# Performance work log

Measured on AMD Instinct MI355X. Metric: run time of the kernel, lower is better.

Reference implementation:

```python
import jax, jax.numpy as jnp
import numpy as np

N_NODES = 50000
N_EDGES_UND = 400000
N_GRAPHS = 128
LATENT = 64
OUT_DIM = 64
NODE_F = 64
EDGE_F = 32
MAX_LV = 3


def setup_inputs() -> dict:
    key = jax.random.key(0)
    ks = jax.random.split(key, 12)
    rng = np.random.default_rng(0)
    # Build consistent directed edge list: each undirected pair (u,v) yields
    # directed edges e (u->v) and e+E_und (v->u); rev maps each to its twin.
    u = rng.integers(0, N_NODES, size=N_EDGES_UND)
    v = rng.integers(0, N_NODES, size=N_EDGES_UND)
    src = jnp.asarray(np.concatenate([u, v]), dtype=jnp.int32)
    dst = jnp.asarray(np.concatenate([v, u]), dtype=jnp.int32)
    e = np.arange(N_EDGES_UND)
    rev = jnp.asarray(np.concatenate([e + N_EDGES_UND, e]), dtype=jnp.int32)
    graph_ids = jnp.sort(jax.random.randint(ks[0], (N_NODES,), 0, N_GRAPHS)).astype(jnp.int32)
    s = 0.05
    return {
        'node_feat': jax.random.normal(ks[1], (N_NODES, NODE_F), jnp.float32),
        'edge_feat': jax.random.normal(ks[2], (2 * N_EDGES_UND, EDGE_F), jnp.float32),
        'src': src, 'dst': dst, 'rev': rev,
        'graph_ids': graph_ids, 'n_graphs': N_GRAPHS,
        'Wn': jax.random.normal(ks[3], (NODE_F, LATENT), jnp.float32) * s,
        'bn': jnp.zeros((LATENT,), jnp.float32),
        'We': jax.random.normal(ks[4], (EDGE_F, LATENT), jnp.float32) * s,
        'be': jnp.zeros((LATENT,), jnp.float32),
        'Wc': jax.random.normal(ks[5], (LATENT, LATENT), jnp.float32) * s,
        'bc': jnp.zeros((LATENT,), jnp.float32),
        'Wo': jax.random.normal(ks[6], (LATENT, OUT_DIM), jnp.float32) * s,
        'bo': jnp.zeros((OUT_DIM,), jnp.float32),
    }


def reference(node_feat, edge_feat, src, dst, rev, graph_ids, n_graphs,
              Wn, bn, We, be, Wc, bc, Wo, bo):
    n_nodes = node_feat.shape[0]
    # w_n2l / w_e2l
    input_node_linear = node_feat @ Wn + bn                  # [N, D]
    input_edge_linear = edge_feat @ We + be                  # [E, D]
    # n2e spmm: each directed edge gathers its source node's row
    input_message = input_edge_linear + input_node_linear[src]  # [E, D]
    cur = jax.nn.relu(input_message)
    # loopy BP: e2e spmm = (sum of messages into src node) - reverse-edge message
    for _ in range(MAX_LV):
        node_agg = jax.ops.segment_sum(cur, dst, num_segments=n_nodes)  # [N, D]
        e2epool = node_agg[src] - cur[rev]                              # [E, D]
        cur = jax.nn.relu(e2epool @ Wc + bc + input_message)
    # e2n spmm: sum incoming edge messages per node
    e2npool = jax.ops.segment_sum(cur, dst, num_segments=n_nodes)       # [N, D]
    hidden_msg = jax.nn.relu(e2npool)
    reluact = jax.nn.relu(hidden_msg @ Wo + bo)                         # [N, out]
    # subg spmm: sum node outputs per graph
    y = jax.ops.segment_sum(reluact, graph_ids, num_segments=n_graphs)  # [G, out]
    return jax.nn.relu(y)
```

## Files before the change

kernel.cpp:

```cpp
#include <hip/hip_runtime.h>


#define NN 50000
#define NE 800000
#define NG 128
#define D 64
#define LDE 36
#define LDW 66
#define LDO 72

typedef unsigned short u16;
typedef unsigned int u32;
typedef __bf16 bf16x8 __attribute__((ext_vector_type(8)));
typedef float f32x4 __attribute__((ext_vector_type(4)));

__device__ __forceinline__ float b2f(u16 u){ u32 x=((u32)u)<<16; float f; __builtin_memcpy(&f,&x,4); return f; }
__device__ __forceinline__ u16 f2b(float f){ u32 x; __builtin_memcpy(&x,&f,4); x += 0x7fffu + ((x>>16)&1u); return (u16)(x>>16); }
__device__ __forceinline__ u32 pack2(float a, float b){ return (u32)f2b(a) | ((u32)f2b(b)<<16); }
__device__ __forceinline__ void unpack8(uint4 v, float* o){
  o[0]=b2f((u16)(v.x&0xffffu)); o[1]=b2f((u16)(v.x>>16));
  o[2]=b2f((u16)(v.y&0xffffu)); o[3]=b2f((u16)(v.y>>16));
  o[4]=b2f((u16)(v.z&0xffffu)); o[5]=b2f((u16)(v.z>>16));
  o[6]=b2f((u16)(v.w&0xffffu)); o[7]=b2f((u16)(v.w>>16));
}

__global__ __launch_bounds__(256) void k_inl(const float* __restrict__ nf, const float* __restrict__ Wn,
                                             const float* __restrict__ bn, u16* __restrict__ inlb){
  __shared__ float w[D*D];
  for (int i=threadIdx.x;i<D*D;i+=256) w[i]=Wn[i];
  __syncthreads();
  const int d = threadIdx.x&63;
  const int n = blockIdx.x*4 + (threadIdx.x>>6);
  if (n>=NN) return;
  float v = bn[d];
  const float* row = nf + (size_t)n*D;
  #pragma unroll 8
  for (int k=0;k<D;k++) v += row[k]*w[k*D+d];
  inlb[(size_t)n*D+d] = f2b(v);
}

__global__ __launch_bounds__(256) void k_im(const float* __restrict__ ef, const float* __restrict__ We,
                                            const float* __restrict__ be, const u16* __restrict__ inlb,
                                            const int* __restrict__ src, const int* __restrict__ perm,
                                            u16* __restrict__ imP){
  __shared__ __align__(16) u16 efs[64*LDE];
  __shared__ __align__(16) u16 wts[64*LDE];
  __shared__ float os[64*68];
  const int t = threadIdx.x;
  const int ebase = blockIdx.x*64;
  {
    int n=t&63, k0=(t>>6)*8;
    #pragma unroll
    for (int j=0;j<8;j++) wts[n*LDE + k0 + j] = f2b(We[(k0+j)*D + n]);
  }
  {
    int e=t>>2, k0=(t&3)*8;
    const float* p = ef + (size_t)(ebase+e)*32 + k0;
    float4 v0=*(const float4*)p, v1=*(const float4*)(p+4);
    uint4 pk = make_uint4(pack2(v0.x,v0.y),pack2(v0.z,v0.w),pack2(v1.x,v1.y),pack2(v1.z,v1.w));
    *(uint4*)&efs[e*LDE + k0] = pk;
  }
  __syncthreads();
  {
    int w=t>>6, lane=t&63, q=lane>>4, mr=lane&15;
    int rowb=w*16;
    bf16x8 A = *(const bf16x8*)&efs[(rowb+mr)*LDE + q*8];
    #pragma unroll
    for (int nt=0;nt<4;nt++){
      bf16x8 B = *(const bf16x8*)&wts[(nt*16+mr)*LDE + q*8];
      f32x4 acc = {0.f,0.f,0.f,0.f};
      acc = __builtin_amdgcn_mfma_f32_16x16x32_bf16(A,B,acc,0,0,0);
      #pragma unroll
      for (int r=0;r<4;r++) os[(rowb+q*4+r)*68 + nt*16+mr] = acc[r];
    }
  }
  __syncthreads();
  {
    int e=t>>2, d0=(t&3)*16;
    const size_t eg = (size_t)(ebase+e);
    const int s = src[eg], ps = perm[eg];
    const u16* ip = inlb + (size_t)s*D + d0;
    uint4 iv0 = *(const uint4*)ip, iv1 = *(const uint4*)(ip+8);
    float il[16]; unpack8(iv0,il); unpack8(iv1,il+8);
    float x[16];
    #pragma unroll
    for (int j=0;j<16;j++) x[j] = os[e*68 + d0 + j] + be[d0+j] + il[j];
    uint4 p0 = make_uint4(pack2(x[0],x[1]),pack2(x[2],x[3]),pack2(x[4],x[5]),pack2(x[6],x[7]));
    uint4 p1 = make_uint4(pack2(x[8],x[9]),pack2(x[10],x[11]),pack2(x[12],x[13]),pack2(x[14],x[15]));
    u16* op = imP + (size_t)ps*D + d0;
    *(uint4*)op = p0; *(uint4*)(op+8) = p1;
  }
}

template<int MODE>
__global__ __launch_bounds__(256) void k_iter(const u16* __restrict__ imP, const u16* __restrict__ revIn,
      const float* __restrict__ naW_in, const float* __restrict__ Wc, const float* __restrict__ bc,
      const int* __restrict__ srcP, const int* __restrict__ prevP, const int* __restrict__ nodeP,
      u16* __restrict__ revOut, float* __restrict__ naW_out){
  __shared__ __align__(16) u16 xs[64*LDW];
  __shared__ __align__(16) u16 wts[64*LDW];
  __shared__ __align__(16) u16 os[64*LDO];
  __shared__ int nid[64];
  const int t = threadIdx.x;
  const size_t sbase = (size_t)blockIdx.x*64;
  {
    int n=t&63, k0=(t>>6)*16;
    #pragma unroll
    for (int j=0;j<16;j++) wts[n*LDW + k0 + j] = f2b(Wc[(k0+j)*D + n]);
  }
  if (t < 64) nid[t] = nodeP[sbase + t];
  {
    const int e = t>>2, d0 = (t&3)*16;
    const size_t slot = sbase + e;
    const u16* ip = imP + slot*D + d0;
    uint4 r0 = *(const uint4*)ip;
    uint4 r1 = *(const uint4*)(ip+8);
    float x[16];
    unpack8(r0, x); unpack8(r1, x+8);
    if (MODE == 1){
      const int sp = srcP[slot];
      const u16* cp = revIn + slot*D + d0;
      uint4 c0 = *(const uint4*)cp, c1 = *(const uint4*)(cp+8);
      const float* np_ = naW_in + (size_t)sp*D + d0;
      float4 a0=*(const float4*)np_,     a1=*(const float4*)(np_+4);
      float4 a2=*(const float4*)(np_+8), a3=*(const float4*)(np_+12);
      float nv[16] = {a0.x,a0.y,a0.z,a0.w, a1.x,a1.y,a1.z,a1.w,
                      a2.x,a2.y,a2.z,a2.w, a3.x,a3.y,a3.z,a3.w};
      float cv[16];
      unpack8(c0,cv); unpack8(c1,cv+8);
      #pragma unroll
      for (int j=0;j<16;j++) x[j] += nv[j] - cv[j] + bc[d0+j];
    }
    #pragma unroll
    for (int j=0;j<16;j++) x[j] = x[j]>0.f ? x[j] : 0.f;
    uint4 p0 = make_uint4(pack2(x[0],x[1]),pack2(x[2],x[3]),pack2(x[4],x[5]),pack2(x[6],x[7]));
    uint4 p1 = make_uint4(pack2(x[8],x[9]),pack2(x[10],x[11]),pack2(x[12],x[13]),pack2(x[14],x[15]));
    u16* q = &xs[e*LDW + d0];
    *(uint4*)q = p0; *(uint4*)(q+8) = p1;
  }
  __syncthreads();
  {
    const int w=t>>6, lane=t&63, q=lane>>4, mr=lane&15;
    const int rowb = w*16;
    bf16x8 A0 = *(const bf16x8*)&xs[(rowb+mr)*LDW + q*8];
    bf16x8 A1 = *(const bf16x8*)&xs[(rowb+mr)*LDW + 32 + q*8];
    #pragma unroll
    for (int nt=0;nt<4;nt++){
      bf16x8 B0 = *(const bf16x8*)&wts[(nt*16+mr)*LDW + q*8];
      bf16x8 B1 = *(const bf16x8*)&wts[(nt*16+mr)*LDW + 32 + q*8];
      f32x4 acc = {0.f,0.f,0.f,0.f};
      acc = __builtin_amdgcn_mfma_f32_16x16x32_bf16(A0,B0,acc,0,0,0);
      acc = __builtin_amdgcn_mfma_f32_16x16x32_bf16(A1,B1,acc,0,0,0);
      #pragma unroll
      for (int r=0;r<4;r++) os[(rowb+q*4+r)*LDO + nt*16 + mr] = f2b(acc[r]);
    }
    const int lr = lane>>2, cc = lane&3;
    const int tgt = prevP[sbase + rowb + lr];
    u16* gp = revOut + (size_t)tgt*D + cc*16;
    *(uint4*)gp     = *(const uint4*)&os[(rowb+lr)*LDO + cc*16];
    *(uint4*)(gp+8) = *(const uint4*)&os[(rowb+lr)*LDO + cc*16 + 8];
    const int d = lane;
    float acc = 0.f;
    int curn = nid[rowb];
    #pragma unroll 4
    for (int r = rowb; r < rowb+16; ++r){
      int n = nid[r];
      if (n != curn){
        atomicAdd(&naW_out[(size_t)curn*D + d], acc);
        curn = n; acc = 0.f;
      }
      acc += b2f(os[r*LDO + d]);
    }
    atomicAdd(&naW_out[(size_t)curn*D + d], acc);
  }
}

__global__ __launch_bounds__(256) void k_last(const u16* __restrict__ imP, const u16* __restrict__ revIn,
      const float* __restrict__ naW_in, const float* __restrict__ bc,
      const int* __restrict__ srcP, const int* __restrict__ nodeP,
      float* __restrict__ e2n){
  __shared__ __align__(16) u16 xs[64*LDW];
  __shared__ int nid[64];
  const int t = threadIdx.x;
  const size_t sbase = (size_t)blockIdx.x*64;
  if (t < 64) nid[t] = nodeP[sbase + t];
  {
    const int e = t>>2, d0 = (t&3)*16;
    const size_t slot = sbase + e;
    const u16* ip = imP + slot*D + d0;
    uint4 r0 = *(const uint4*)ip, r1 = *(const uint4*)(ip+8);
    float x[16];
    unpack8(r0, x); unpack8(r1, x+8);
    const int sp = srcP[slot];
    const u16* cp = revIn + slot*D + d0;
    uint4 c0 = *(const uint4*)cp, c1 = *(const uint4*)(cp+8);
    const float* np_ = naW_in + (size_t)sp*D + d0;
    float4 a0=*(const float4*)np_,     a1=*(const float4*)(np_+4);
    float4 a2=*(const float4*)(np_+8), a3=*(const float4*)(np_+12);
    float nv[16] = {a0.x,a0.y,a0.z,a0.w, a1.x,a1.y,a1.z,a1.w,
                    a2.x,a2.y,a2.z,a2.w, a3.x,a3.y,a3.z,a3.w};
    float cv[16];
    unpack8(c0,cv); unpack8(c1,cv+8);
    #pragma unroll
    for (int j=0;j<16;j++){ x[j] += nv[j] - cv[j] + bc[d0+j]; x[j] = x[j]>0.f ? x[j] : 0.f; }
    uint4 p0 = make_uint4(pack2(x[0],x[1]),pack2(x[2],x[3]),pack2(x[4],x[5]),pack2(x[6],x[7]));
    uint4 p1 = make_uint4(pack2(x[8],x[9]),pack2(x[10],x[11]),pack2(x[12],x[13]),pack2(x[14],x[15]));
    u16* q = &xs[e*LDW + d0];
    *(uint4*)q = p0; *(uint4*)(q+8) = p1;
  }
  __syncthreads();
  {
    const int d = t&63, g = t>>6;
    float acc = 0.f;
    int curn = nid[g*16];
    #pragma unroll 4
    for (int r = g*16; r < g*16+16; ++r){
      int n = nid[r];
      if (n != curn){
        atomicAdd(&e2n[(size_t)curn*D + d], acc);
        curn = n; acc = 0.f;
      }
      acc += b2f(xs[r*LDW + d]);
    }
    atomicAdd(&e2n[(size_t)curn*D + d], acc);
  }
}

__global__ void k_hist(const int* __restrict__ dst, int* __restrict__ cnt){
  int e = blockIdx.x*256 + threadIdx.x;
  atomicAdd(&cnt[dst[e]], 1);
}
__global__ __launch_bounds__(1024) void k_scan1(const int* __restrict__ cnt, int* __restrict__ outv,
                                                int* __restrict__ bsums, int n){
  __shared__ int sh[1024];
  int i = blockIdx.x*1024 + threadIdx.x;
  int v = (i<n)? cnt[i] : 0;
  sh[threadIdx.x]=v;
  __syncthreads();
  for (int off=1; off<1024; off<<=1){
    int tv = (threadIdx.x>=(unsigned)off)? sh[threadIdx.x-off] : 0;
    __syncthreads();
    sh[threadIdx.x] += tv;
    __syncthreads();
  }
  if (i<n) outv[i] = sh[threadIdx.x] - v;
  if (threadIdx.x==1023) bsums[blockIdx.x] = sh[1023];
}
__global__ void k_scan2(int* bsums, int nb, int* tot){
  if (threadIdx.x==0 && blockIdx.x==0){
    int run=0;
    for (int b=0;b<nb;b++){ int v=bsums[b]; bsums[b]=run; run+=v; }
    *tot = run;
  }
}
__global__ __launch_bounds__(1024) void k_scan3(int* __restrict__ off, int* __restrict__ cur,
                                                const int* __restrict__ bsums, int n){
  int i = blockIdx.x*1024 + threadIdx.x;
  if (i<n){ int v = off[i] + bsums[blockIdx.x]; off[i]=v; cur[i]=v; }
}
__global__ void k_fill(const int* __restrict__ dst, const int* __restrict__ src,
                       int* __restrict__ cur, int* __restrict__ perm,
                       int* __restrict__ srcP, int* __restrict__ nodeP){
  int e = blockIdx.x*256 + threadIdx.x;
  int d = dst[e];
  int pos = atomicAdd(&cur[d], 1);
  perm[e] = pos;
  srcP[pos] = src[e];
  nodeP[pos] = d;
}
__global__ void k_prev(const int* __restrict__ rev, const int* __restrict__ perm, int* __restrict__ prevP){
  int e = blockIdx.x*256 + threadIdx.x;
  prevP[perm[e]] = perm[rev[e]];
}

__global__ __launch_bounds__(256) void k_final(const float* __restrict__ e2n, const float* __restrict__ Wo,
                                               const float* __restrict__ bo, const int* __restrict__ gid,
                                               float* __restrict__ yacc){
  __shared__ float w[D*D];
  for (int i=threadIdx.x;i<D*D;i+=256) w[i]=Wo[i];
  __syncthreads();
  const int d = threadIdx.x&63, sub = threadIdx.x>>6;
  const int n0 = blockIdx.x*32 + sub*8;
  const float bod = bo[d];
  float acc=0.f; int curg=-1;
  for (int i=0;i<8;i++){
    int n=n0+i;
    if (n>=NN) break;
    int g = gid[n];
    if (g!=curg){ if (curg>=0) atomicAdd(&yacc[curg*D+d], acc); curg=g; acc=0.f; }
    float v=bod;
    const float* er = e2n + (size_t)n*D;
    #pragma unroll 8
    for (int k=0;k<D;k++){ float h=er[k]; h = h>0.f?h:0.f; v += h*w[k*D+d]; }
    acc += (v>0.f ? v : 0.f);
  }
  if (curg>=0) atomicAdd(&yacc[curg*D+d], acc);
}
__global__ void k_out(const float* __restrict__ yacc, float* __restrict__ outp){
  int i = blockIdx.x*256 + threadIdx.x;
  if (i<NG*D){ float v=yacc[i]; outp[i]= v>0.f?v:0.f; }
}

static constexpr size_t SZ_E   = (size_t)NE*D*2;
static constexpr size_t SZ_NF4 = (size_t)NN*D*4;
static constexpr size_t SZ_NB  = (size_t)NN*D*2;
static constexpr size_t OFF_IMP  = 0;
static constexpr size_t OFF_RVA  = SZ_E;
static constexpr size_t OFF_RVB  = 2*SZ_E;
static constexpr size_t OFF_NA0  = 3*SZ_E;
static constexpr size_t OFF_NA1  = OFF_NA0 + SZ_NF4;
static constexpr size_t OFF_E2N  = OFF_NA1 + SZ_NF4;
static constexpr size_t OFF_INL  = OFF_E2N + SZ_NF4;
static constexpr size_t OFF_COFF = OFF_INL + SZ_NB;
static constexpr size_t OFF_CCUR = OFF_COFF + 200064;
static constexpr size_t OFF_PERM = OFF_CCUR + 200064;
static constexpr size_t OFF_SRCP = OFF_PERM + (size_t)NE*4;
static constexpr size_t OFF_PRVP = OFF_SRCP + (size_t)NE*4;
static constexpr size_t OFF_NODP = OFF_PRVP + (size_t)NE*4;
static constexpr size_t OFF_BS   = OFF_NODP + (size_t)NE*4;
static constexpr size_t OFF_YACC = OFF_BS + 256;

extern "C" void kernel_launch(void* const* d_in, const int* in_sizes, int n_in,
                              void* d_out, int out_size, void* d_ws, size_t ws_size,
                              hipStream_t stream) {
  const float* node_feat = (const float*)d_in[0];
  const float* edge_feat = (const float*)d_in[1];
  const int*   src       = (const int*)d_in[2];
  const int*   dst       = (const int*)d_in[3];
  const int*   rev       = (const int*)d_in[4];
  const int*   gid       = (const int*)d_in[5];
  const float* Wn = (const float*)d_in[7];
  const float* bn = (const float*)d_in[8];
  const float* We = (const float*)d_in[9];
  const float* be = (const float*)d_in[10];
  const float* Wc = (const float*)d_in[11];
  const float* bc = (const float*)d_in[12];
  const float* Wo = (const float*)d_in[13];
  const float* bo = (const float*)d_in[14];

  char* ws = (char*)d_ws;
  u16*   imP     = (u16*)(ws + OFF_IMP);
  u16*   revA    = (u16*)(ws + OFF_RVA);
  u16*   revB    = (u16*)(ws + OFF_RVB);
  float* naW0    = (float*)(ws + OFF_NA0);
  float* naW1    = (float*)(ws + OFF_NA1);
  float* e2n     = (float*)(ws + OFF_E2N);
  u16*   inlb    = (u16*)(ws + OFF_INL);
  int*   csr_off = (int*)(ws + OFF_COFF);
  int*   csr_cur = (int*)(ws + OFF_CCUR);
  int*   perm    = (int*)(ws + OFF_PERM);
  int*   srcP    = (int*)(ws + OFF_SRCP);
  int*   prevP   = (int*)(ws + OFF_PRVP);
  int*   nodeP   = (int*)(ws + OFF_NODP);
  int*   bsums   = (int*)(ws + OFF_BS);
  float* yacc    = (float*)(ws + OFF_YACC);

  hipMemsetAsync(csr_cur, 0, NN*sizeof(int), stream);
  hipMemsetAsync(yacc, 0, NG*D*sizeof(float), stream);

  k_hist <<<NE/256, 256, 0, stream>>>(dst, csr_cur);
  k_scan1<<<49, 1024, 0, stream>>>(csr_cur, csr_off, bsums, NN);
  k_scan2<<<1, 64, 0, stream>>>(bsums, 49, csr_off + NN);
  k_scan3<<<49, 1024, 0, stream>>>(csr_off, csr_cur, bsums, NN);
  k_fill <<<NE/256, 256, 0, stream>>>(dst, src, csr_cur, perm, srcP, nodeP);
  k_prev <<<NE/256, 256, 0, stream>>>(rev, perm, prevP);

  k_inl<<<NN/4, 256, 0, stream>>>(node_feat, Wn, bn, inlb);
  k_im <<<NE/64, 256, 0, stream>>>(edge_feat, We, be, inlb, src, perm, imP);

  hipMemsetAsync(naW0, 0, SZ_NF4, stream);
  k_iter<0><<<NE/64, 256, 0, stream>>>(imP, revA, naW0, Wc, bc, srcP, prevP, nodeP, revA, naW0);
  hipMemsetAsync(naW1, 0, SZ_NF4, stream);
  k_iter<1><<<NE/64, 256, 0, stream>>>(imP, revA, naW0, Wc, bc, srcP, prevP, nodeP, revB, naW1);
  hipMemsetAsync(naW0, 0, SZ_NF4, stream);
  k_iter<1><<<NE/64, 256, 0, stream>>>(imP, revB, naW1, Wc, bc, srcP, prevP, nodeP, revA, naW0);
  hipMemsetAsync(e2n, 0, SZ_NF4, stream);
  k_last<<<NE/64, 256, 0, stream>>>(imP, revA, naW0, bc, srcP, nodeP, e2n);

  k_final<<<(NN+31)/32, 256, 0, stream>>>(e2n, Wo, bo, gid, yacc);
  k_out<<<(NG*D)/256, 256, 0, stream>>>(yacc, (float*)d_out);
}
```

Before: 710.3 us.

## Pretranspose weights, bf16 node aggregates, multi-tile iter blocks, merge memsets and scans

Weights Wc and We are transposed and converted to bf16 once in a prep kernel instead of in every block. Each k_iter block now processes four 64-edge tiles, amortising the weight staging. The fp32 node aggregates are converted to a bf16 copy before each gather, halving the bytes of the random reads. Several memsets are merged into one by reordering the workspace, k_scan2 is folded into k_scan3 with a wave reduction, and some barriers are removed because each wave now uses only its own rows. This adds extra conversion kernels, lowers the precision of the aggregates, and the removed barrier in k_im is questionable: each thread reads os rows written by other waves' MFMA results.

```diff
diff --git a/kernel.cpp b/kernel.cpp
--- a/kernel.cpp
+++ b/kernel.cpp
@@ -24,6 +24,23 @@
   o[6]=b2f((u16)(v.w&0xffffu)); o[7]=b2f((u16)(v.w>>16));
 }
 
+__global__ __launch_bounds__(256) void k_prep(const float* __restrict__ Wc, const float* __restrict__ We,
+                                              u16* __restrict__ wcT, u16* __restrict__ weT){
+  int i = blockIdx.x*256 + threadIdx.x;
+  if (i < 4096){ int n=i>>6, k=i&63; wcT[i] = f2b(Wc[k*D+n]); }
+  int j = i - 4096;
+  if (j >= 0 && j < 2048){ int n=j>>5, k=j&31; weT[j] = f2b(We[k*D+n]); }
+}
+
+template<int ZERO>
+__global__ __launch_bounds__(256) void k_cvt(const float* __restrict__ srcv, u16* __restrict__ dstb,
+                                             float* __restrict__ zbuf){
+  size_t i = (size_t)(blockIdx.x*256 + threadIdx.x)*4;
+  float4 v = *(const float4*)(srcv + i);
+  *(uint2*)(dstb + i) = make_uint2(pack2(v.x,v.y), pack2(v.z,v.w));
+  if (ZERO) *(float4*)(zbuf + i) = make_float4(0.f,0.f,0.f,0.f);
+}
+
 __global__ __launch_bounds__(256) void k_inl(const float* __restrict__ nf, const float* __restrict__ Wn,
                                              const float* __restrict__ bn, u16* __restrict__ inlb){
   __shared__ float w[D*D];
@@ -39,7 +56,7 @@
   inlb[(size_t)n*D+d] = f2b(v);
 }
 
-__global__ __launch_bounds__(256) void k_im(const float* __restrict__ ef, const float* __restrict__ We,
+__global__ __launch_bounds__(256) void k_im(const float* __restrict__ ef, const u16* __restrict__ weT,
                                             const float* __restrict__ be, const u16* __restrict__ inlb,
                                             const int* __restrict__ src, const int* __restrict__ perm,
                                             u16* __restrict__ imP){
@@ -50,8 +67,7 @@
   const int ebase = blockIdx.x*64;
   {
     int n=t&63, k0=(t>>6)*8;
-    #pragma unroll
-    for (int j=0;j<8;j++) wts[n*LDE + k0 + j] = f2b(We[(k0+j)*D + n]);
+    *(uint4*)&wts[n*LDE + k0] = *(const uint4*)(weT + n*32 + k0);
   }
   {
     int e=t>>2, k0=(t&3)*8;
@@ -74,7 +90,6 @@
       for (int r=0;r<4;r++) os[(rowb+q*4+r)*68 + nt*16+mr] = acc[r];
     }
   }
-  __syncthreads();
   {
     int e=t>>2, d0=(t&3)*16;
     const size_t eg = (size_t)(ebase+e);
@@ -94,7 +109,7 @@
 
 template<int MODE>
 __global__ __launch_bounds__(256) void k_iter(const u16* __restrict__ imP, const u16* __restrict__ revIn,
-      const float* __restrict__ naW_in, const float* __restrict__ Wc, const float* __restrict__ bc,
+      const u16* __restrict__ naWb, const u16* __restrict__ wcT, const float* __restrict__ bc,
       const int* __restrict__ srcP, const int* __restrict__ prevP, const int* __restrict__ nodeP,
       u16* __restrict__ revOut, float* __restrict__ naW_out){
   __shared__ __align__(16) u16 xs[64*LDW];
@@ -102,127 +117,129 @@
   __shared__ __align__(16) u16 os[64*LDO];
   __shared__ int nid[64];
   const int t = threadIdx.x;
-  const size_t sbase = (size_t)blockIdx.x*64;
-  {
-    int n=t&63, k0=(t>>6)*16;
-    #pragma unroll
-    for (int j=0;j<16;j++) wts[n*LDW + k0 + j] = f2b(Wc[(k0+j)*D + n]);
-  }
-  if (t < 64) nid[t] = nodeP[sbase + t];
-  {
-    const int e = t>>2, d0 = (t&3)*16;
-    const size_t slot = sbase + e;
-    const u16* ip = imP + slot*D + d0;
-    uint4 r0 = *(const uint4*)ip;
-    uint4 r1 = *(const uint4*)(ip+8);
-    float x[16];
-    unpack8(r0, x); unpack8(r1, x+8);
-    if (MODE == 1){
-      const int sp = srcP[slot];
-      const u16* cp = revIn + slot*D + d0;
-      uint4 c0 = *(const uint4*)cp, c1 = *(const uint4*)(cp+8);
-      const float* np_ = naW_in + (size_t)sp*D + d0;
-      float4 a0=*(const float4*)np_,     a1=*(const float4*)(np_+4);
-      float4 a2=*(const float4*)(np_+8), a3=*(const float4*)(np_+12);
-      float nv[16] = {a0.x,a0.y,a0.z,a0.w, a1.x,a1.y,a1.z,a1.w,
-                      a2.x,a2.y,a2.z,a2.w, a3.x,a3.y,a3.z,a3.w};
-      float cv[16];
-      unpack8(c0,cv); unpack8(c1,cv+8);
+  const int lane = t&63, w = t>>6;
+  {
+    const int k0 = w*16;
+    *(uint4*)&wts[lane*LDW + k0]     = *(const uint4*)(wcT + lane*64 + k0);
+    *(uint4*)&wts[lane*LDW + k0 + 8] = *(const uint4*)(wcT + lane*64 + k0 + 8);
+  }
+  const int e = t>>2, d0 = (t&3)*16;
+  float bcr[16];
+  if (MODE == 1){
+    float4 b0=*(const float4*)(bc+d0),   b1=*(const float4*)(bc+d0+4);
+    float4 b2=*(const float4*)(bc+d0+8), b3=*(const float4*)(bc+d0+12);
+    bcr[0]=b0.x;bcr[1]=b0.y;bcr[2]=b0.z;bcr[3]=b0.w; bcr[4]=b1.x;bcr[5]=b1.y;bcr[6]=b1.z;bcr[7]=b1.w;
+    bcr[8]=b2.x;bcr[9]=b2.y;bcr[10]=b2.z;bcr[11]=b2.w; bcr[12]=b3.x;bcr[13]=b3.y;bcr[14]=b3.z;bcr[15]=b3.w;
+  }
+  __syncthreads();
+  const int q = lane>>4, mr = lane&15;
+  const int rowb = w*16;
+  #pragma unroll 1
+  for (int tile=0; tile<4; ++tile){
+    const size_t tbase = (size_t)blockIdx.x*256 + (size_t)tile*64;
+    if (lane < 16) nid[rowb + lane] = nodeP[tbase + rowb + lane];
+    {
+      const size_t slot = tbase + e;
+      const u16* ip = imP + slot*D + d0;
+      uint4 r0 = *(const uint4*)ip, r1 = *(const uint4*)(ip+8);
+      float x[16]; unpack8(r0,x); unpack8(r1,x+8);
+      if (MODE == 1){
+        const int sp = srcP[slot];
+        const u16* cp = revIn + slot*D + d0;
+        uint4 c0=*(const uint4*)cp, c1=*(const uint4*)(cp+8);
+        const u16* np_ = naWb + (size_t)sp*D + d0;
+        uint4 n0=*(const uint4*)np_, n1=*(const uint4*)(np_+8);
+        float cv[16], nv[16];
+        unpack8(c0,cv); unpack8(c1,cv+8);
+        unpack8(n0,nv); unpack8(n1,nv+8);
+        #pragma unroll
+        for (int j=0;j<16;j++) x[j] += nv[j] - cv[j] + bcr[j];
+      }
       #pragma unroll
-      for (int j=0;j<16;j++) x[j] += nv[j] - cv[j] + bc[d0+j];
+      for (int j=0;j<16;j++) x[j] = x[j]>0.f ? x[j] : 0.f;
+      uint4 p0 = make_uint4(pack2(x[0],x[1]),pack2(x[2],x[3]),pack2(x[4],x[5]),pack2(x[6],x[7]));
+      uint4 p1 = make_uint4(pack2(x[8],x[9]),pack2(x[10],x[11]),pack2(x[12],x[13]),pack2(x[14],x[15]));
+      u16* qd = &xs[e*LDW + d0];
+      *(uint4*)qd = p0; *(uint4*)(qd+8) = p1;
     }
-    #pragma unroll
-    for (int j=0;j<16;j++) x[j] = x[j]>0.f ? x[j] : 0.f;
-    uint4 p0 = make_uint4(pack2(x[0],x[1]),pack2(x[2],x[3]),pack2(x[4],x[5]),pack2(x[6],x[7]));
-    uint4 p1 = make_uint4(pack2(x[8],x[9]),pack2(x[10],x[11]),pack2(x[12],x[13]),pack2(x[14],x[15]));
-    u16* q = &xs[e*LDW + d0];
-    *(uint4*)q = p0; *(uint4*)(q+8) = p1;
-  }
-  __syncthreads();
-  {
-    const int w=t>>6, lane=t&63, q=lane>>4, mr=lane&15;
-    const int rowb = w*16;
-    bf16x8 A0 = *(const bf16x8*)&xs[(rowb+mr)*LDW + q*8];
-    bf16x8 A1 = *(const bf16x8*)&xs[(rowb+mr)*LDW + 32 + q*8];
-    #pragma unroll
-    for (int nt=0;nt<4;nt++){
-      bf16x8 B0 = *(const bf16x8*)&wts[(nt*16+mr)*LDW + q*8];
-      bf16x8 B1 = *(const bf16x8*)&wts[(nt*16+mr)*LDW + 32 + q*8];
-      f32x4 acc = {0.f,0.f,0.f,0.f};
-      acc = __builtin_amdgcn_mfma_f32_16x16x32_bf16(A0,B0,acc,0,0,0);
-      acc = __builtin_amdgcn_mfma_f32_16x16x32_bf16(A1,B1,acc,0,0,0);
+    {
+      bf16x8 A0 = *(const bf16x8*)&xs[(rowb+mr)*LDW + q*8];
+      bf16x8 A1 = *(const bf16x8*)&xs[(rowb+mr)*LDW + 32 + q*8];
       #pragma unroll
-      for (int r=0;r<4;r++) os[(rowb+q*4+r)*LDO + nt*16 + mr] = f2b(acc[r]);
+      for (int nt=0;nt<4;nt++){
+        bf16x8 B0 = *(const bf16x8*)&wts[(nt*16+mr)*LDW + q*8];
+        bf16x8 B1 = *(const bf16x8*)&wts[(nt*16+mr)*LDW + 32 + q*8];
+        f32x4 acc = {0.f,0.f,0.f,0.f};
+        acc = __builtin_amdgcn_mfma_f32_16x16x32_bf16(A0,B0,acc,0,0,0);
+        acc = __builtin_amdgcn_mfma_f32_16x16x32_bf16(A1,B1,acc,0,0,0);
+        #pragma unroll
+        for (int r=0;r<4;r++) os[(rowb+q*4+r)*LDO + nt*16 + mr] = f2b(acc[r]);
+      }
+      const int lr = lane>>2, cc = lane&3;
+      const int tgt = prevP[tbase + rowb + lr];
+      u16* gp = revOut + (size_t)tgt*D + cc*16;
+      *(uint4*)gp     = *(const uint4*)&os[(rowb+lr)*LDO + cc*16];
+      *(uint4*)(gp+8) = *(const uint4*)&os[(rowb+lr)*LDO + cc*16 + 8];
+      float acc = 0.f;
+      int curn = nid[rowb];
+      #pragma unroll 4
+      for (int i=0;i<16;++i){
+        int n = nid[rowb+i];
+        if (n != curn){
+          atomicAdd(&naW_out[(size_t)curn*D + lane], acc);
+          curn = n; acc = 0.f;
+        }
+        acc += b2f(os[(rowb+i)*LDO + lane]);
+      }
+      atomicAdd(&naW_out[(size_t)curn*D + lane], acc);
     }
-    const int lr = lane>>2, cc = lane&3;
-    const int tgt = prevP[sbase + rowb + lr];
-    u16* gp = revOut + (size_t)tgt*D + cc*16;
-    *(uint4*)gp     = *(const uint4*)&os[(rowb+lr)*LDO + cc*16];
-    *(uint4*)(gp+8) = *(const uint4*)&os[(rowb+lr)*LDO + cc*16 + 8];
-    const int d = lane;
-    float acc = 0.f;
-    int curn = nid[rowb];
-    #pragma unroll 4
-    for (int r = rowb; r < rowb+16; ++r){
-      int n = nid[r];
-      if (n != curn){
-        atomicAdd(&naW_out[(size_t)curn*D + d], acc);
-        curn = n; acc = 0.f;
-      }
-      acc += b2f(os[r*LDO + d]);
-    }
-    atomicAdd(&naW_out[(size_t)curn*D + d], acc);
   }
 }
 
 __global__ __launch_bounds__(256) void k_last(const u16* __restrict__ imP, const u16* __restrict__ revIn,
-      const float* __restrict__ naW_in, const float* __restrict__ bc,
+      const u16* __restrict__ naWb, const float* __restrict__ bc,
       const int* __restrict__ srcP, const int* __restrict__ nodeP,
       float* __restrict__ e2n){
   __shared__ __align__(16) u16 xs[64*LDW];
   __shared__ int nid[64];
   const int t = threadIdx.x;
+  const int lane = t&63, w = t>>6;
   const size_t sbase = (size_t)blockIdx.x*64;
-  if (t < 64) nid[t] = nodeP[sbase + t];
+  if (lane < 16) nid[w*16+lane] = nodeP[sbase + w*16 + lane];
   {
     const int e = t>>2, d0 = (t&3)*16;
     const size_t slot = sbase + e;
     const u16* ip = imP + slot*D + d0;
     uint4 r0 = *(const uint4*)ip, r1 = *(const uint4*)(ip+8);
-    float x[16];
-    unpack8(r0, x); unpack8(r1, x+8);
+    float x[16]; unpack8(r0,x); unpack8(r1,x+8);
     const int sp = srcP[slot];
     const u16* cp = revIn + slot*D + d0;
     uint4 c0 = *(const uint4*)cp, c1 = *(const uint4*)(cp+8);
-    const float* np_ = naW_in + (size_t)sp*D + d0;
-    float4 a0=*(const float4*)np_,     a1=*(const float4*)(np_+4);
-    float4 a2=*(const float4*)(np_+8), a3=*(const float4*)(np_+12);
-    float nv[16] = {a0.x,a0.y,a0.z,a0.w, a1.x,a1.y,a1.z,a1.w,
-                    a2.x,a2.y,a2.z,a2.w, a3.x,a3.y,a3.z,a3.w};
-    float cv[16];
+    const u16* np_ = naWb + (size_t)sp*D + d0;
+    uint4 n0 = *(const uint4*)np_, n1 = *(const uint4*)(np_+8);
+    float cv[16], nv[16];
     unpack8(c0,cv); unpack8(c1,cv+8);
+    unpack8(n0,nv); unpack8(n1,nv+8);
     #pragma unroll
     for (int j=0;j<16;j++){ x[j] += nv[j] - cv[j] + bc[d0+j]; x[j] = x[j]>0.f ? x[j] : 0.f; }
     uint4 p0 = make_uint4(pack2(x[0],x[1]),pack2(x[2],x[3]),pack2(x[4],x[5]),pack2(x[6],x[7]));
     uint4 p1 = make_uint4(pack2(x[8],x[9]),pack2(x[10],x[11]),pack2(x[12],x[13]),pack2(x[14],x[15]));
-    u16* q = &xs[e*LDW + d0];
-    *(uint4*)q = p0; *(uint4*)(q+8) = p1;
-  }
-  __syncthreads();
-  {
-    const int d = t&63, g = t>>6;
+    u16* qd = &xs[e*LDW + d0];
+    *(uint4*)qd = p0; *(uint4*)(qd+8) = p1;
+  }
+  {
     float acc = 0.f;
-    int curn = nid[g*16];
+    int curn = nid[w*16];
     #pragma unroll 4
-    for (int r = g*16; r < g*16+16; ++r){
-      int n = nid[r];
+    for (int i=0;i<16;++i){
+      int n = nid[w*16+i];
       if (n != curn){
-        atomicAdd(&e2n[(size_t)curn*D + d], acc);
+        atomicAdd(&e2n[(size_t)curn*D + lane], acc);
         curn = n; acc = 0.f;
       }
-      acc += b2f(xs[r*LDW + d]);
+      acc += b2f(xs[(w*16+i)*LDW + lane]);
     }
-    atomicAdd(&e2n[(size_t)curn*D + d], acc);
+    atomicAdd(&e2n[(size_t)curn*D + lane], acc);
   }
 }
 
@@ -246,17 +263,18 @@
   if (i<n) outv[i] = sh[threadIdx.x] - v;
   if (threadIdx.x==1023) bsums[blockIdx.x] = sh[1023];
 }
-__global__ void k_scan2(int* bsums, int nb, int* tot){
-  if (threadIdx.x==0 && blockIdx.x==0){
-    int run=0;
-    for (int b=0;b<nb;b++){ int v=bsums[b]; bsums[b]=run; run+=v; }
-    *tot = run;
-  }
-}
 __global__ __launch_bounds__(1024) void k_scan3(int* __restrict__ off, int* __restrict__ cur,
                                                 const int* __restrict__ bsums, int n){
+  __shared__ int spref;
+  if (threadIdx.x < 64){
+    int v = ((int)threadIdx.x < (int)blockIdx.x) ? bsums[threadIdx.x] : 0;
+    #pragma unroll
+    for (int o=1;o<64;o<<=1) v += __shfl_xor(v, o, 64);
+    if (threadIdx.x==0) spref = v;
+  }
+  __syncthreads();
   int i = blockIdx.x*1024 + threadIdx.x;
-  if (i<n){ int v = off[i] + bsums[blockIdx.x]; off[i]=v; cur[i]=v; }
+  if (i<n){ int v = off[i] + spref; off[i]=v; cur[i]=v; }
 }
 __global__ void k_fill(const int* __restrict__ dst, const int* __restrict__ src,
                        int* __restrict__ cur, int* __restrict__ perm,
@@ -307,18 +325,22 @@
 static constexpr size_t OFF_IMP  = 0;
 static constexpr size_t OFF_RVA  = SZ_E;
 static constexpr size_t OFF_RVB  = 2*SZ_E;
-static constexpr size_t OFF_NA0  = 3*SZ_E;
+static constexpr size_t OFF_CCUR = 3*SZ_E;
+static constexpr size_t OFF_NA0  = OFF_CCUR + 200064;
 static constexpr size_t OFF_NA1  = OFF_NA0 + SZ_NF4;
 static constexpr size_t OFF_E2N  = OFF_NA1 + SZ_NF4;
-static constexpr size_t OFF_INL  = OFF_E2N + SZ_NF4;
+static constexpr size_t OFF_YACC = OFF_E2N + SZ_NF4;
+static constexpr size_t ZERO_SZ  = 200064 + 3*SZ_NF4 + (size_t)NG*D*4;
+static constexpr size_t OFF_NAB  = OFF_YACC + (size_t)NG*D*4;
+static constexpr size_t OFF_INL  = OFF_NAB + SZ_NB;
 static constexpr size_t OFF_COFF = OFF_INL + SZ_NB;
-static constexpr size_t OFF_CCUR = OFF_COFF + 200064;
-static constexpr size_t OFF_PERM = OFF_CCUR + 200064;
+static constexpr size_t OFF_PERM = OFF_COFF + 200064;
 static constexpr size_t OFF_SRCP = OFF_PERM + (size_t)NE*4;
 static constexpr size_t OFF_PRVP = OFF_SRCP + (size_t)NE*4;
 static constexpr size_t OFF_NODP = OFF_PRVP + (size_t)NE*4;
 static constexpr size_t OFF_BS   = OFF_NODP + (size_t)NE*4;
-static constexpr size_t OFF_YACC = OFF_BS + 256;
+static constexpr size_t OFF_WCT  = OFF_BS + 256;
+static constexpr size_t OFF_WET  = OFF_WCT + 8192;
 
 extern "C" void kernel_launch(void* const* d_in, const int* in_sizes, int n_in,
                               void* d_out, int out_size, void* d_ws, size_t ws_size,
@@ -345,6 +367,8 @@
   float* naW0    = (float*)(ws + OFF_NA0);
   float* naW1    = (float*)(ws + OFF_NA1);
   float* e2n     = (float*)(ws + OFF_E2N);
+  float* yacc    = (float*)(ws + OFF_YACC);
+  u16*   naWb    = (u16*)(ws + OFF_NAB);
   u16*   inlb    = (u16*)(ws + OFF_INL);
   int*   csr_off = (int*)(ws + OFF_COFF);
   int*   csr_cur = (int*)(ws + OFF_CCUR);
@@ -353,29 +377,28 @@
   int*   prevP   = (int*)(ws + OFF_PRVP);
   int*   nodeP   = (int*)(ws + OFF_NODP);
   int*   bsums   = (int*)(ws + OFF_BS);
-  float* yacc    = (float*)(ws + OFF_YACC);
-
-  hipMemsetAsync(csr_cur, 0, NN*sizeof(int), stream);
-  hipMemsetAsync(yacc, 0, NG*D*sizeof(float), stream);
+  u16*   wcT     = (u16*)(ws + OFF_WCT);
+  u16*   weT     = (u16*)(ws + OFF_WET);
+
+  hipMemsetAsync(ws + OFF_CCUR, 0, ZERO_SZ, stream);
 
   k_hist <<<NE/256, 256, 0, stream>>>(dst, csr_cur);
   k_scan1<<<49, 1024, 0, stream>>>(csr_cur, csr_off, bsums, NN);
-  k_scan2<<<1, 64, 0, stream>>>(bsums, 49, csr_off + NN);
   k_scan3<<<49, 1024, 0, stream>>>(csr_off, csr_cur, bsums, NN);
   k_fill <<<NE/256, 256, 0, stream>>>(dst, src, csr_cur, perm, srcP, nodeP);
   k_prev <<<NE/256, 256, 0, stream>>>(rev, perm, prevP);
 
-  k_inl<<<NN/4, 256, 0, stream>>>(node_feat, Wn, bn, inlb);
-  k_im <<<NE/64, 256, 0, stream>>>(edge_feat, We, be, inlb, src, perm, imP);
-
-  hipMemsetAsync(naW0, 0, SZ_NF4, stream);
-  k_iter<0><<<NE/64, 256, 0, stream>>>(imP, revA, naW0, Wc, bc, srcP, prevP, nodeP, revA, naW0);
-  hipMemsetAsync(naW1, 0, SZ_NF4, stream);
-  k_iter<1><<<NE/64, 256, 0, stream>>>(imP, revA, naW0, Wc, bc, srcP, prevP, nodeP, revB, naW1);
-  hipMemsetAsync(naW0, 0, SZ_NF4, stream);
-  k_iter<1><<<NE/64, 256, 0, stream>>>(imP, revB, naW1, Wc, bc, srcP, prevP, nodeP, revA, naW0);
-  hipMemsetAsync(e2n, 0, SZ_NF4, stream);
-  k_last<<<NE/64, 256, 0, stream>>>(imP, revA, naW0, bc, srcP, nodeP, e2n);
+  k_prep<<<24, 256, 0, stream>>>(Wc, We, wcT, weT);
+  k_inl <<<NN/4, 256, 0, stream>>>(node_feat, Wn, bn, inlb);
+  k_im  <<<NE/64, 256, 0, stream>>>(edge_feat, weT, be, inlb, src, perm, imP);
+
+  k_iter<0><<<NE/256, 256, 0, stream>>>(imP, revA, naWb, wcT, bc, srcP, prevP, nodeP, revA, naW0);
+  k_cvt<0><<<3125, 256, 0, stream>>>(naW0, naWb, (float*)nullptr);
+  k_iter<1><<<NE/256, 256, 0, stream>>>(imP, revA, naWb, wcT, bc, srcP, prevP, nodeP, revB, naW1);
+  k_cvt<1><<<3125, 256, 0, stream>>>(naW1, naWb, naW0);
+  k_iter<1><<<NE/256, 256, 0, stream>>>(imP, revB, naWb, wcT, bc, srcP, prevP, nodeP, revA, naW0);
+  k_cvt<0><<<3125, 256, 0, stream>>>(naW0, naWb, (float*)nullptr);
+  k_last<<<NE/64, 256, 0, stream>>>(imP, revA, naWb, bc, srcP, nodeP, e2n);
 
   k_final<<<(NN+31)/32, 256, 0, stream>>>(e2n, Wo, bo, gid, yacc);
   k_out<<<(NG*D)/256, 256, 0, stream>>>(yacc, (float*)d_out);
```

Result: no change. 711.8 us (+0.2%).
